# Performance work log

Hardware: AMD Instinct MI355X
Metric: run time of the kernel (lower is better)

Reference implementation:

```python
import jax, jax.numpy as jnp
import numpy as np
import math

B, L, DIM = 2, 2048, 1024
HEADS = 16
DH = DIM // HEADS  # 64
M_IALSH = 2
U_IALSH = 0.75
NEG = -1e4  # additive mask value for non-matching hash buckets


def setup_inputs() -> dict:
    key = jax.random.key(0)
    k0, k1, k2, k3 = jax.random.split(key, 4)
    return {
        "hidden_states": jax.random.normal(k0, (B, L, DIM), jnp.float32),
        "qk_w": jax.random.normal(k1, (DIM, DIM), jnp.float32) * 0.02,
        "qk_b": jnp.zeros((DIM,), jnp.float32),
        "v_w": jax.random.normal(k2, (DIM, DIM), jnp.float32) * 0.02,
        "v_b": jnp.zeros((DIM,), jnp.float32),
        "hash_a": jax.random.normal(k3, (DH + M_IALSH,), jnp.float32),
    }


def _ialsh_mask(qkh, hash_a):
    # qkh: (b, h, l, dh). IALSH (Improved Asymmetric LSH for MIPS):
    # keys scaled so max norm per (b,h) is U; P(x)=[x, 1/2-||x||^2, 1/2-||x||^4]
    # queries unit-normalized;        Q(x)=[x/||x||, 0, 0]
    norms = jnp.linalg.norm(qkh, axis=-1, keepdims=True)          # (b,h,l,1)
    max_norm = jnp.max(norms, axis=2, keepdims=True)              # (b,h,1,1)
    xk = qkh * (U_IALSH / jnp.maximum(max_norm, 1e-12))
    nk2 = jnp.sum(xk * xk, axis=-1, keepdims=True)                # ||x||^2
    P = jnp.concatenate([xk, 0.5 - nk2, 0.5 - nk2 * nk2], axis=-1)
    q_unit = qkh / jnp.maximum(norms, 1e-12)
    zeros = jnp.zeros_like(nk2)
    Q = jnp.concatenate([q_unit, zeros, zeros], axis=-1)
    hq = (Q @ hash_a) >= 0.0                                      # (b,h,l) sign hash
    hk = (P @ hash_a) >= 0.0
    same = hq[..., :, None] == hk[..., None, :]                   # (b,h,l,l)
    return jnp.where(same, 0.0, NEG).astype(qkh.dtype)


def reference(hidden_states, qk_w, qk_b, v_w, v_b, hash_a):
    b, l, d = hidden_states.shape
    qk = hidden_states @ qk_w.T + qk_b                            # shared Q/K projection
    v = hidden_states @ v_w.T + v_b

    def split(x):  # (b,l,d) -> (b,h,l,dh)
        return x.reshape(b, l, HEADS, DH).transpose(0, 2, 1, 3)

    qkh, vh = split(qk), split(v)
    scores = jnp.einsum('bhqd,bhkd->bhqk', qkh, qkh) / math.sqrt(DH)
    scores = scores + _ialsh_mask(qkh, hash_a)
    probs = jax.nn.softmax(scores, axis=-1)  # dropout = identity (eval mode)
    ctx = jnp.einsum('bhqk,bhkd->bhqd', probs, vh)
    return ctx.transpose(0, 2, 1, 3).reshape(b, l, d)
```

## Files before the change

### kernel.cpp

```cpp
#include <hip/hip_runtime.h>

typedef unsigned short u16;
typedef unsigned char  u8;
typedef unsigned int   u32;

typedef short bf16x8 __attribute__((ext_vector_type(8)));
typedef float f32x4  __attribute__((ext_vector_type(4)));

#define DEV __device__ __forceinline__

#if __has_builtin(__builtin_amdgcn_exp2f)
#define EXP2(x) __builtin_amdgcn_exp2f(x)
#else
#define EXP2(x) exp2f(x)
#endif

DEV u16 f2bf(float x) {
  u32 u = __builtin_bit_cast(u32, x);
  u32 r = (u + 0x7fffu + ((u >> 16) & 1u)) >> 16;
  return (u16)r;
}
DEV float bf2f(u16 h) {
  u32 u = ((u32)h) << 16;
  return __builtin_bit_cast(float, u);
}
DEV f32x4 mfma16(bf16x8 a, bf16x8 b, f32x4 c) {
  return __builtin_amdgcn_mfma_f32_16x16x32_bf16(a, b, c, 0, 0, 0);
}

#define GLDS(gptr, lptr)                                                  \
  __builtin_amdgcn_global_load_lds(                                       \
      (const __attribute__((address_space(1))) void*)(gptr),              \
      (__attribute__((address_space(3))) void*)(lptr), 16, 0, 0)

__global__ __launch_bounds__(256) void split3_kernel(
    const float* __restrict__ hid, const float* __restrict__ wq,
    const float* __restrict__ wv,
    u16* __restrict__ hHi, u16* __restrict__ hLo,
    u16* __restrict__ wqHi, u16* __restrict__ wqLo, u16* __restrict__ wvHi) {
  const int NH = 4194304, NW = 1048576;
  int i = blockIdx.x * 256 + threadIdx.x;
  if (i < NH) {
    float v = hid[i];
    u16 t = f2bf(v);
    hHi[i] = t;
    hLo[i] = f2bf(v - bf2f(t));
  } else if (i < NH + NW) {
    int j = i - NH;
    float v = wq[j];
    u16 t = f2bf(v);
    wqHi[j] = t;
    wqLo[j] = f2bf(v - bf2f(t));
  } else {
    int j = i - NH - NW;
    wvHi[j] = f2bf(wv[j]);
  }
}

__global__ __launch_bounds__(256) void ca_kernel(
    const float* __restrict__ W, const float* __restrict__ ha, double* __restrict__ ca) {
  int idx = blockIdx.x * 256 + threadIdx.x;
  int h = idx >> 10, k = idx & 1023;
  double s = 0.0;
#pragma unroll 8
  for (int j = 0; j < 64; ++j)
    s += (double)W[(size_t)(h * 64 + j) * 1024 + k] * (double)ha[j];
  ca[idx] = s;
}

__global__ __launch_bounds__(256) void d_kernel(
    const float* __restrict__ hid, const double* __restrict__ ca, float* __restrict__ dq) {
  const int row  = blockIdx.x * 4 + (threadIdx.x >> 6);
  const int lane = threadIdx.x & 63;
  const int b = row >> 11, l = row & 2047;
  double acc[16];
#pragma unroll
  for (int h = 0; h < 16; ++h) acc[h] = 0.0;
  const float* hp = hid + (size_t)row * 1024;
  for (int k = lane; k < 1024; k += 64) {
    const double hv = (double)hp[k];
#pragma unroll
    for (int h = 0; h < 16; ++h) acc[h] += hv * ca[h * 1024 + k];
  }
#pragma unroll
  for (int h = 0; h < 16; ++h) {
    double v = acc[h];
#pragma unroll
    for (int off = 32; off; off >>= 1) v += __shfl_xor(v, off, 64);
    if (lane == 0) dq[(size_t)(b * 16 + h) * 2048 + l] = (float)v;
  }
}

__global__ __launch_bounds__(256, 2) void gemm_fused(
    const u16* __restrict__ hHi, const u16* __restrict__ hLo,
    const u16* __restrict__ wqHi, const u16* __restrict__ wqLo,
    const u16* __restrict__ wvHi,
    const float* __restrict__ qk_b, const float* __restrict__ v_b,
    u16* __restrict__ qkB, u16* __restrict__ vT, float* __restrict__ n2A) {
  constexpr int K = 1024;
  __shared__ u16 S[2][16384];
  const int tid = threadIdx.x, wave = tid >> 6, lane = tid & 63;
  const int quad = lane >> 4, lm = lane & 15;
  const int wr = wave >> 1, wc = wave & 1;
  const int m0 = blockIdx.x * 64, n0 = blockIdx.y * 128;
  const int ch = lane & 3, rA = lane >> 2;

  auto stage = [&](int kt, int buf) {
    const int k0 = kt * 32;
    const int rowA = wave * 16 + rA;
    GLDS(hHi + (size_t)(m0 + rowA) * K + k0 + ch * 8, &S[buf][0 + wave * 512]);
    GLDS(hLo + (size_t)(m0 + rowA) * K + k0 + ch * 8, &S[buf][2048 + wave * 512]);
#pragma unroll
    for (int it = 0; it < 2; ++it) {
      const int rb = wave * 2 + it;
      const int row = rb * 16 + rA;
      GLDS(wqHi + (size_t)(n0 + row) * K + k0 + ch * 8, &S[buf][4096 + rb * 512]);
      GLDS(wqLo + (size_t)(n0 + row) * K + k0 + ch * 8, &S[buf][8192 + rb * 512]);
      GLDS(wvHi + (size_t)(n0 + row) * K + k0 + ch * 8, &S[buf][12288 + rb * 512]);
    }
  };

  f32x4 aq[2][4], av[4][2];
#pragma unroll
  for (int i = 0; i < 2; ++i)
#pragma unroll
    for (int j = 0; j < 4; ++j) aq[i][j] = {0.f, 0.f, 0.f, 0.f};
#pragma unroll
  for (int i = 0; i < 4; ++i)
#pragma unroll
    for (int j = 0; j < 2; ++j) av[i][j] = {0.f, 0.f, 0.f, 0.f};

  stage(0, 0);
  __syncthreads();

  for (int kt = 0; kt < 32; ++kt) {
    const int cur = kt & 1;
    if (kt < 31) stage(kt + 1, cur ^ 1);

    bf16x8 a_h[2], a_l[2], b_h[4], b_l[4], w_h[4];
#pragma unroll
    for (int i = 0; i < 2; ++i) {
      a_h[i] = *(const bf16x8*)&S[cur][(wr * 32 + i * 16 + lm) * 32 + quad * 8];
      a_l[i] = *(const bf16x8*)&S[cur][2048 + (wr * 32 + i * 16 + lm) * 32 + quad * 8];
    }
#pragma unroll
    for (int j = 0; j < 4; ++j) {
      b_h[j] = *(const bf16x8*)&S[cur][4096 + (wc * 64 + j * 16 + lm) * 32 + quad * 8];
      b_l[j] = *(const bf16x8*)&S[cur][8192 + (wc * 64 + j * 16 + lm) * 32 + quad * 8];
      w_h[j] = *(const bf16x8*)&S[cur][12288 + (wc * 64 + j * 16 + lm) * 32 + quad * 8];
    }
#pragma unroll
    for (int i = 0; i < 2; ++i)
#pragma unroll
      for (int j = 0; j < 4; ++j) {
        aq[i][j] = mfma16(a_h[i], b_h[j], aq[i][j]);
        aq[i][j] = mfma16(a_h[i], b_l[j], aq[i][j]);
        aq[i][j] = mfma16(a_l[i], b_h[j], aq[i][j]);
      }
#pragma unroll
    for (int iv = 0; iv < 4; ++iv)
#pragma unroll
      for (int jv = 0; jv < 2; ++jv)
        av[iv][jv] = mfma16(w_h[iv], a_h[jv], av[iv][jv]);

    __syncthreads();
  }

  const int hidx = blockIdx.y * 2 + wc;
#pragma unroll
  for (int i = 0; i < 2; ++i) {
    float nn[4] = {0.f, 0.f, 0.f, 0.f};
#pragma unroll
    for (int j = 0; j < 4; ++j) {
      const int col = n0 + wc * 64 + j * 16 + lm;
      const float bv = qk_b[col];
#pragma unroll
      for (int r = 0; r < 4; ++r) {
        const int row = m0 + wr * 32 + i * 16 + quad * 4 + r;
        const float val = aq[i][j][r] + bv;
        qkB[(size_t)row * 1024 + col] = f2bf(val);
        nn[r] += val * val;
      }
    }
#pragma unroll
    for (int r = 0; r < 4; ++r)
#pragma unroll
      for (int off = 1; off < 16; off <<= 1) nn[r] += __shfl_xor(nn[r], off, 64);
    if (lm == 0) {
      const int row = m0 + wr * 32 + i * 16 + quad * 4;
      const int b = row >> 11, l = row & 2047;
      *(float4*)&n2A[(size_t)(b * 16 + hidx) * 2048 + l] =
          make_float4(nn[0], nn[1], nn[2], nn[3]);
    }
  }
#pragma unroll
  for (int iv = 0; iv < 4; ++iv)
#pragma unroll
    for (int r = 0; r < 4; ++r) {
      const int vcol = n0 + wc * 64 + iv * 16 + quad * 4 + r;
      const float bv = v_b[vcol];
#pragma unroll
      for (int jv = 0; jv < 2; ++jv) {
        const int tok = m0 + wr * 32 + jv * 16 + lm;
        vT[(size_t)vcol * 4096 + tok] = f2bf(av[iv][jv][r] + bv);
      }
    }
}

__global__ __launch_bounds__(256) void bits_kernel(
    const float* __restrict__ n2A, const float* __restrict__ dq,
    const float* __restrict__ ha, u8* __restrict__ hqA, u8* __restrict__ hkA) {
  const int bh = blockIdx.x;
  const int tid = threadIdx.x;
  const int wave = tid >> 6, lane = tid & 63;
  __shared__ float red[4];
  const float* n2p = n2A + (size_t)bh * 2048;
  float4 v0 = ((const float4*)n2p)[tid];
  float4 v1 = ((const float4*)n2p)[tid + 256];
  float lmax = fmaxf(fmaxf(fmaxf(v0.x, v0.y), fmaxf(v0.z, v0.w)),
                     fmaxf(fmaxf(v1.x, v1.y), fmaxf(v1.z, v1.w)));
#pragma unroll
  for (int off = 1; off < 64; off <<= 1) lmax = fmaxf(lmax, __shfl_xor(lmax, off, 64));
  if (lane == 0) red[wave] = lmax;
  __syncthreads();
  const float maxn2 = fmaxf(fmaxf(red[0], red[1]), fmaxf(red[2], red[3]));
  const float s = 0.75f / fmaxf(sqrtf(maxn2), 1e-12f);
  const float a64 = ha[64], a65 = ha[65];
#pragma unroll
  for (int it = 0; it < 8; ++it) {
    const int l = it * 256 + tid;
    const float dv = dq[(size_t)bh * 2048 + l];
    const float n2 = n2p[l];
    const float nk2 = s * s * n2;
    const float hkdot = s * dv + (0.5f - nk2) * a64 + (0.5f - nk2 * nk2) * a65;
    hqA[(size_t)bh * 2048 + l] = (dv >= 0.f) ? 1 : 0;
    hkA[(size_t)bh * 2048 + l] = (hkdot >= 0.f) ? 1 : 0;
  }
}

__global__ __launch_bounds__(256, 4) void attn_kernel(
    const u16* __restrict__ qkb, const u16* __restrict__ vT,
    const u8* __restrict__ hqA, const u8* __restrict__ hkA, float* __restrict__ out) {
  __shared__ u16 Ks[2][4096];
  __shared__ u16 Vs[2][4096];
  __shared__ u16 Ps[4][1024];

  const int qt = blockIdx.x;
  const int bh = blockIdx.y;
  const int b = bh >> 4, h = bh & 15;
  const int tid = threadIdx.x, wave = tid >> 6, lane = tid & 63;
  const int quad = lane >> 4, lm = lane & 15;
  const int lx = lm & 7;
  const int r8 = lane >> 3, ch = lane & 7;
  const int q0 = qt * 64;

  const u16* qbase = qkb + (size_t)b * 2048 * 1024 + h * 64;
  const u16* vtb = vT + (size_t)h * 64 * 4096 + b * 2048;
  const u8* hkp = hkA + (size_t)bh * 2048;

  bf16x8 aQ[2];
#pragma unroll
  for (int c = 0; c < 2; ++c)
    aQ[c] = *(const bf16x8*)(qbase +
        (size_t)(q0 + wave * 16 + lm) * 1024 + c * 32 + quad * 8);
  u8 hqb[4];
  {
    const u8* hqp = hqA + (size_t)bh * 2048 + q0 + wave * 16;
#pragma unroll
    for (int r = 0; r < 4; ++r) hqb[r] = hqp[quad * 4 + r];
  }

  const int srow = wave * 16;
  auto stage = [&](int kt, int buf) {
#pragma unroll
    for (int i = 0; i < 2; ++i) {
      const int row = srow + i * 8 + r8;
      const int sw = (ch ^ (row & 7)) * 8;
      GLDS(qbase + (size_t)(kt * 64 + row) * 1024 + sw, &Ks[buf][(srow + i * 8) * 64]);
      GLDS(vtb + (size_t)row * 4096 + kt * 64 + sw, &Vs[buf][(srow + i * 8) * 64]);
    }
  };

  stage(0, 0);

  f32x4 acc_o[4], accL;
  accL = {0.f, 0.f, 0.f, 0.f};
#pragma unroll
  for (int j = 0; j < 4; ++j) acc_o[j] = {0.f, 0.f, 0.f, 0.f};
  const bf16x8 ones = {0x3F80, 0x3F80, 0x3F80, 0x3F80, 0x3F80, 0x3F80, 0x3F80, 0x3F80};
  const float SCL = 0.18033688f;
  const float M0 = -4.3280854f;
  const float M1 = -1.4430768e4f;

  __syncthreads();

  for (int kt = 0; kt < 32; ++kt) {
    const int cur = kt & 1;
    if (kt < 31) stage(kt + 1, cur ^ 1);

    u8 hkv[4];
#pragma unroll
    for (int nb = 0; nb < 4; ++nb) hkv[nb] = hkp[kt * 64 + nb * 16 + lm];

    f32x4 cs[4];
#pragma unroll
    for (int nb = 0; nb < 4; ++nb) cs[nb] = {0.f, 0.f, 0.f, 0.f};
#pragma unroll
    for (int c = 0; c < 2; ++c)
#pragma unroll
      for (int nb = 0; nb < 4; ++nb) {
        bf16x8 bK = *(const bf16x8*)&Ks[cur][(nb * 16 + lm) * 64 + (((c * 4 + quad) ^ lx) * 8)];
        cs[nb] = mfma16(aQ[c], bK, cs[nb]);
      }

#pragma unroll
    for (int nb = 0; nb < 4; ++nb)
#pragma unroll
      for (int r = 0; r < 4; ++r) {
        const float msel = (hqb[r] == hkv[nb]) ? M0 : M1;
        const float p = EXP2(__builtin_fmaf(cs[nb][r], SCL, msel));
        const int prow = quad * 4 + r;
        const int pc = (nb * 2 + (lm >> 3)) ^ (prow & 7);
        union { float f; u16 hw[2]; } u;
        u.f = p;
        Ps[wave][prow * 64 + pc * 8 + lx] = u.hw[1];
      }

    bf16x8 aP[2];
#pragma unroll
    for (int c = 0; c < 2; ++c) {
      aP[c] = *(const bf16x8*)&Ps[wave][lm * 64 + (((c * 4 + quad) ^ lx) * 8)];
      accL = mfma16(aP[c], ones, accL);
    }
#pragma unroll
    for (int c = 0; c < 2; ++c)
#pragma unroll
      for (int j = 0; j < 4; ++j) {
        bf16x8 bV = *(const bf16x8*)&Vs[cur][(j * 16 + lm) * 64 + (((c * 4 + quad) ^ lx) * 8)];
        acc_o[j] = mfma16(aP[c], bV, acc_o[j]);
      }

    __syncthreads();
  }

#pragma unroll
  for (int r = 0; r < 4; ++r) {
    const float inv = 1.0f / accL[r];
    float* op = out + (size_t)(b * 2048 + q0 + wave * 16 + quad * 4 + r) * 1024 + h * 64;
#pragma unroll
    for (int j = 0; j < 4; ++j) op[j * 16 + lm] = acc_o[j][r] * inv;
  }
}

extern "C" void kernel_launch(void* const* d_in, const int* in_sizes, int n_in,
                              void* d_out, int out_size, void* d_ws, size_t ws_size,
                              hipStream_t stream) {
  const float* hidden = (const float*)d_in[0];
  const float* qk_w   = (const float*)d_in[1];
  const float* qk_b   = (const float*)d_in[2];
  const float* v_w    = (const float*)d_in[3];
  const float* v_b    = (const float*)d_in[4];
  const float* hash_a = (const float*)d_in[5];
  float* out = (float*)d_out;

  char* base = (char*)d_ws;
  size_t off = 0;
  auto take = [&](size_t bytes) -> char* {
    char* r = base + off;
    off += (bytes + 255) & ~(size_t)255;
    return r;
  };
  const size_t NH = 4194304;
  const size_t NW = 1048576;
  u16* hHi  = (u16*)take(NH * 2);
  u16* hLo  = (u16*)take(NH * 2);
  u16* wqHi = (u16*)take(NW * 2);
  u16* wqLo = (u16*)take(NW * 2);
  u16* wvHi = (u16*)take(NW * 2);
  u16* qkB  = (u16*)take(NH * 2);
  u16* vT   = (u16*)take(NH * 2);
  double* ca = (double*)take(16 * 1024 * 8);
  float* dq  = (float*)take(65536 * 4);
  float* n2A = (float*)take(65536 * 4);
  u8* hqA = (u8*)take(65536);
  u8* hkA = (u8*)take(65536);

  hipLaunchKernelGGL(split3_kernel, dim3((NH + 2 * NW) / 256), dim3(256), 0, stream,
                     hidden, qk_w, v_w, hHi, hLo, wqHi, wqLo, wvHi);
  hipLaunchKernelGGL(ca_kernel, dim3(64), dim3(256), 0, stream, qk_w, hash_a, ca);
  hipLaunchKernelGGL(d_kernel, dim3(1024), dim3(256), 0, stream, hidden, ca, dq);
  hipLaunchKernelGGL(gemm_fused, dim3(64, 8), dim3(256), 0, stream,
                     hHi, hLo, wqHi, wqLo, wvHi, qk_b, v_b, qkB, vT, n2A);
  hipLaunchKernelGGL(bits_kernel, dim3(32), dim3(256), 0, stream, n2A, dq, hash_a, hqA, hkA);
  hipLaunchKernelGGL(attn_kernel, dim3(32, 32), dim3(256), 0, stream, qkB, vT, hqA, hkA, out);
}
```

Baseline: 230.7 us.

## Rewrite attention with 32x32 MFMA, register-resident P, and bitmask hash buckets

The attention kernel now uses 32x32x16 MFMAs, with each wave handling 32 query tokens and a 128-query tile per block. The S tile is computed transposed (K as A operand), so the P fragment is built in registers with cvt_pk_bf16 and permlane32_swap instead of a round trip through LDS. Key hash bits are packed into 64-bit ballot masks, and the mask is applied as a bit select after exp2 instead of a per-element compare and large additive constant. The row sum comes from scalar accumulation rather than an MFMA with ones, the grid is flattened so heads vary fastest, and s_setprio hints are added. Occupancy drops to 2 blocks per CU, and the row sum is now taken from the fp32 probabilities rather than their bf16-rounded values used in the PV product.

```diff
diff --git a/kernel.cpp b/kernel.cpp
--- a/kernel.cpp
+++ b/kernel.cpp
@@ -3,9 +3,11 @@
 typedef unsigned short u16;
 typedef unsigned char  u8;
 typedef unsigned int   u32;
+typedef unsigned long long u64;
 
 typedef short bf16x8 __attribute__((ext_vector_type(8)));
 typedef float f32x4  __attribute__((ext_vector_type(4)));
+typedef float f32x16 __attribute__((ext_vector_type(16)));
 
 #define DEV __device__ __forceinline__
 
@@ -26,6 +28,22 @@
 }
 DEV f32x4 mfma16(bf16x8 a, bf16x8 b, f32x4 c) {
   return __builtin_amdgcn_mfma_f32_16x16x32_bf16(a, b, c, 0, 0, 0);
+}
+DEV f32x16 mfma32(bf16x8 a, bf16x8 b, f32x16 c) {
+  return __builtin_amdgcn_mfma_f32_32x32x16_bf16(a, b, c, 0, 0, 0);
+}
+DEV u32 cvtpk(float lo, float hi) {
+  u32 r;
+  asm("v_cvt_pk_bf16_f32 %0, %1, %2" : "=v"(r) : "v"(lo), "v"(hi));
+  return r;
+}
+DEV void pswap(u32& x, u32& y) {
+  asm("v_permlane32_swap_b32 %0, %1" : "+v"(x), "+v"(y));
+}
+DEV bf16x8 mkfrag(u32 w0, u32 w1, u32 w2, u32 w3) {
+  union { u32 w[4]; bf16x8 v; } u;
+  u.w[0] = w0; u.w[1] = w1; u.w[2] = w2; u.w[3] = w3;
+  return u.v;
 }
 
 #define GLDS(gptr, lptr)                                                  \
@@ -209,7 +227,7 @@
 
 __global__ __launch_bounds__(256) void bits_kernel(
     const float* __restrict__ n2A, const float* __restrict__ dq,
-    const float* __restrict__ ha, u8* __restrict__ hqA, u8* __restrict__ hkA) {
+    const float* __restrict__ ha, u8* __restrict__ hqA, u64* __restrict__ hkM) {
   const int bh = blockIdx.x;
   const int tid = threadIdx.x;
   const int wave = tid >> 6, lane = tid & 63;
@@ -234,41 +252,38 @@
     const float nk2 = s * s * n2;
     const float hkdot = s * dv + (0.5f - nk2) * a64 + (0.5f - nk2 * nk2) * a65;
     hqA[(size_t)bh * 2048 + l] = (dv >= 0.f) ? 1 : 0;
-    hkA[(size_t)bh * 2048 + l] = (hkdot >= 0.f) ? 1 : 0;
-  }
-}
-
-__global__ __launch_bounds__(256, 4) void attn_kernel(
+    const u64 m = __ballot(hkdot >= 0.f);
+    if (lane == 0) hkM[(size_t)bh * 32 + it * 4 + wave] = m;
+  }
+}
+
+__global__ __launch_bounds__(256, 2) void attn_kernel(
     const u16* __restrict__ qkb, const u16* __restrict__ vT,
-    const u8* __restrict__ hqA, const u8* __restrict__ hkA, float* __restrict__ out) {
+    const u8* __restrict__ hqA, const u64* __restrict__ hkM,
+    float* __restrict__ out) {
   __shared__ u16 Ks[2][4096];
   __shared__ u16 Vs[2][4096];
-  __shared__ u16 Ps[4][1024];
-
-  const int qt = blockIdx.x;
-  const int bh = blockIdx.y;
+
+  const int id = blockIdx.x;
+  const int bh = id & 31, qt = id >> 5;
   const int b = bh >> 4, h = bh & 15;
   const int tid = threadIdx.x, wave = tid >> 6, lane = tid & 63;
-  const int quad = lane >> 4, lm = lane & 15;
-  const int lx = lm & 7;
+  const int col = lane & 31;
+  const int hf = lane >> 5;
+  const int ch7 = col & 7;
   const int r8 = lane >> 3, ch = lane & 7;
-  const int q0 = qt * 64;
+  const int q0 = qt * 128;
+  const int token = q0 + wave * 32 + col;
 
   const u16* qbase = qkb + (size_t)b * 2048 * 1024 + h * 64;
   const u16* vtb = vT + (size_t)h * 64 * 4096 + b * 2048;
-  const u8* hkp = hkA + (size_t)bh * 2048;
-
-  bf16x8 aQ[2];
-#pragma unroll
-  for (int c = 0; c < 2; ++c)
-    aQ[c] = *(const bf16x8*)(qbase +
-        (size_t)(q0 + wave * 16 + lm) * 1024 + c * 32 + quad * 8);
-  u8 hqb[4];
-  {
-    const u8* hqp = hqA + (size_t)bh * 2048 + q0 + wave * 16;
-#pragma unroll
-    for (int r = 0; r < 4; ++r) hqb[r] = hqp[quad * 4 + r];
-  }
+  const u64* hkp = hkM + (size_t)bh * 32;
+
+  bf16x8 aQ[4];
+#pragma unroll
+  for (int c = 0; c < 4; ++c)
+    aQ[c] = *(const bf16x8*)(qbase + (size_t)token * 1024 + c * 16 + hf * 8);
+  const u32 hqx = hqA[(size_t)bh * 2048 + token] ? 0xFFFFFFFFu : 0u;
 
   const int srow = wave * 16;
   auto stage = [&](int kt, int buf) {
@@ -281,75 +296,92 @@
     }
   };
 
-  stage(0, 0);
-
-  f32x4 acc_o[4], accL;
-  accL = {0.f, 0.f, 0.f, 0.f};
-#pragma unroll
-  for (int j = 0; j < 4; ++j) acc_o[j] = {0.f, 0.f, 0.f, 0.f};
-  const bf16x8 ones = {0x3F80, 0x3F80, 0x3F80, 0x3F80, 0x3F80, 0x3F80, 0x3F80, 0x3F80};
+  f32x16 acc[2];
+#pragma unroll
+  for (int d = 0; d < 2; ++d)
+#pragma unroll
+    for (int r = 0; r < 16; ++r) acc[d][r] = 0.f;
+  float accL = 0.f;
+
   const float SCL = 0.18033688f;
   const float M0 = -4.3280854f;
-  const float M1 = -1.4430768e4f;
-
+
+  u64 mk = hkp[0];
+  stage(0, 0);
   __syncthreads();
 
   for (int kt = 0; kt < 32; ++kt) {
     const int cur = kt & 1;
     if (kt < 31) stage(kt + 1, cur ^ 1);
-
-    u8 hkv[4];
-#pragma unroll
-    for (int nb = 0; nb < 4; ++nb) hkv[nb] = hkp[kt * 64 + nb * 16 + lm];
-
-    f32x4 cs[4];
-#pragma unroll
-    for (int nb = 0; nb < 4; ++nb) cs[nb] = {0.f, 0.f, 0.f, 0.f};
-#pragma unroll
-    for (int c = 0; c < 2; ++c)
-#pragma unroll
-      for (int nb = 0; nb < 4; ++nb) {
-        bf16x8 bK = *(const bf16x8*)&Ks[cur][(nb * 16 + lm) * 64 + (((c * 4 + quad) ^ lx) * 8)];
-        cs[nb] = mfma16(aQ[c], bK, cs[nb]);
-      }
-
-#pragma unroll
-    for (int nb = 0; nb < 4; ++nb)
-#pragma unroll
-      for (int r = 0; r < 4; ++r) {
-        const float msel = (hqb[r] == hkv[nb]) ? M0 : M1;
-        const float p = EXP2(__builtin_fmaf(cs[nb][r], SCL, msel));
-        const int prow = quad * 4 + r;
-        const int pc = (nb * 2 + (lm >> 3)) ^ (prow & 7);
-        union { float f; u16 hw[2]; } u;
-        u.f = p;
-        Ps[wave][prow * 64 + pc * 8 + lx] = u.hw[1];
-      }
-
-    bf16x8 aP[2];
-#pragma unroll
-    for (int c = 0; c < 2; ++c) {
-      aP[c] = *(const bf16x8*)&Ps[wave][lm * 64 + (((c * 4 + quad) ^ lx) * 8)];
-      accL = mfma16(aP[c], ones, accL);
-    }
-#pragma unroll
-    for (int c = 0; c < 2; ++c)
-#pragma unroll
-      for (int j = 0; j < 4; ++j) {
-        bf16x8 bV = *(const bf16x8*)&Vs[cur][(j * 16 + lm) * 64 + (((c * 4 + quad) ^ lx) * 8)];
-        acc_o[j] = mfma16(aP[c], bV, acc_o[j]);
-      }
-
+    const u64 mk_next = (kt < 31) ? hkp[kt + 1] : 0ull;
+
+    const u64 msh = mk >> (hf * 4);
+    u32 mw[2];
+    mw[0] = (u32)msh;
+    mw[1] = (u32)(msh >> 32);
+
+#pragma unroll
+    for (int kb = 0; kb < 2; ++kb) {
+      const u32 hw = mw[kb] ^ hqx;
+      f32x16 cs;
+#pragma unroll
+      for (int r = 0; r < 16; ++r) cs[r] = 0.f;
+      __builtin_amdgcn_s_setprio(1);
+#pragma unroll
+      for (int c = 0; c < 4; ++c) {
+        const bf16x8 aK = *(const bf16x8*)
+            &Ks[cur][(kb * 32 + col) * 64 + (((c * 2 + hf) ^ ch7) * 8)];
+        cs = mfma32(aK, aQ[c], cs);
+      }
+      __builtin_amdgcn_s_setprio(0);
+
+      float pv[16];
+#pragma unroll
+      for (int r = 0; r < 16; ++r) {
+        const int pos = (r & 3) + 8 * (r >> 2);
+        float p = EXP2(__builtin_fmaf(cs[r], SCL, M0));
+        p = ((hw >> pos) & 1u) ? 0.f : p;
+        accL += p;
+        pv[r] = p;
+      }
+      u32 pk[8];
+#pragma unroll
+      for (int i = 0; i < 8; ++i) pk[i] = cvtpk(pv[2 * i], pv[2 * i + 1]);
+      pswap(pk[0], pk[2]);
+      pswap(pk[1], pk[3]);
+      pswap(pk[4], pk[6]);
+      pswap(pk[5], pk[7]);
+      const bf16x8 fr0 = mkfrag(pk[0], pk[1], pk[2], pk[3]);
+      const bf16x8 fr1 = mkfrag(pk[4], pk[5], pk[6], pk[7]);
+
+      __builtin_amdgcn_s_setprio(1);
+#pragma unroll
+      for (int db = 0; db < 2; ++db) {
+        const bf16x8 aV0 = *(const bf16x8*)
+            &Vs[cur][(db * 32 + col) * 64 + ((((kb * 2 + 0) * 2 + hf) ^ ch7) * 8)];
+        acc[db] = mfma32(aV0, fr0, acc[db]);
+        const bf16x8 aV1 = *(const bf16x8*)
+            &Vs[cur][(db * 32 + col) * 64 + ((((kb * 2 + 1) * 2 + hf) ^ ch7) * 8)];
+        acc[db] = mfma32(aV1, fr1, acc[db]);
+      }
+      __builtin_amdgcn_s_setprio(0);
+    }
+
+    mk = mk_next;
     __syncthreads();
   }
 
-#pragma unroll
-  for (int r = 0; r < 4; ++r) {
-    const float inv = 1.0f / accL[r];
-    float* op = out + (size_t)(b * 2048 + q0 + wave * 16 + quad * 4 + r) * 1024 + h * 64;
-#pragma unroll
-    for (int j = 0; j < 4; ++j) op[j * 16 + lm] = acc_o[j][r] * inv;
-  }
+  accL += __shfl_xor(accL, 32);
+  const float inv = 1.0f / accL;
+  float* op = out + (size_t)(b * 2048 + token) * 1024 + h * 64 + hf * 4;
+#pragma unroll
+  for (int db = 0; db < 2; ++db)
+#pragma unroll
+    for (int g = 0; g < 4; ++g) {
+      float4 v4 = make_float4(acc[db][g * 4 + 0] * inv, acc[db][g * 4 + 1] * inv,
+                              acc[db][g * 4 + 2] * inv, acc[db][g * 4 + 3] * inv);
+      *(float4*)(op + db * 32 + g * 8) = v4;
+    }
 }
 
 extern "C" void kernel_launch(void* const* d_in, const int* in_sizes, int n_in,
@@ -383,7 +415,7 @@
   float* dq  = (float*)take(65536 * 4);
   float* n2A = (float*)take(65536 * 4);
   u8* hqA = (u8*)take(65536);
-  u8* hkA = (u8*)take(65536);
+  u64* hkM = (u64*)take(32 * 32 * 8);
 
   hipLaunchKernelGGL(split3_kernel, dim3((NH + 2 * NW) / 256), dim3(256), 0, stream,
                      hidden, qk_w, v_w, hHi, hLo, wqHi, wqLo, wvHi);
@@ -391,6 +423,6 @@
   hipLaunchKernelGGL(d_kernel, dim3(1024), dim3(256), 0, stream, hidden, ca, dq);
   hipLaunchKernelGGL(gemm_fused, dim3(64, 8), dim3(256), 0, stream,
                      hHi, hLo, wqHi, wqLo, wvHi, qk_b, v_b, qkB, vT, n2A);
-  hipLaunchKernelGGL(bits_kernel, dim3(32), dim3(256), 0, stream, n2A, dq, hash_a, hqA, hkA);
-  hipLaunchKernelGGL(attn_kernel, dim3(32, 32), dim3(256), 0, stream, qkB, vT, hqA, hkA, out);
-}
+  hipLaunchKernelGGL(bits_kernel, dim3(32), dim3(256), 0, stream, n2A, dq, hash_a, hqA, hkM);
+  hipLaunchKernelGGL(attn_kernel, dim3(512), dim3(256), 0, stream, qkB, vT, hqA, hkM, out);
+}
```

After: 228.6 us. No clear change (-0.9%).
